# Kernel optimization log

Measured on AMD Instinct MI355X. Metric: run time of the kernel, lower is better.

Reference implementation:

```python
import jax, jax.numpy as jnp
import numpy as np

N_CLASSES = 16384
M = 2
D = 128


def setup_inputs() -> dict:
    key = jax.random.key(0)
    k1, k2 = jax.random.split(key)
    x = jax.random.normal(k1, (N_CLASSES * M, D), dtype=jnp.float32)
    anchor_idx = jax.random.randint(k2, (N_CLASSES,), 0, M, dtype=jnp.int64 if jax.config.jax_enable_x64 else jnp.int32).astype(jnp.int32)
    pos_idx = (1 - anchor_idx).astype(jnp.int32)  # randperm(2) -> positive is the other sample
    return {"x": x, "anchor_idx": anchor_idx, "pos_idx": pos_idx}


def reference(x, anchor_idx, pos_idx):
    # x: [N*M, D]; anchor_idx/pos_idx: [N] in [0, M)
    N = anchor_idx.shape[0]
    Dx = x.shape[1]
    xr = x.reshape(N, M, Dx)
    anchors = jnp.take_along_axis(xr, anchor_idx[:, None, None], axis=1)[:, 0, :]    # [N, D]
    positives = jnp.take_along_axis(xr, pos_idx[:, None, None], axis=1)[:, 0, :]     # [N, D]
    negs = xr[:, 1, :]                                                               # [N, D] (sample 1 of every class)
    # score[i, j] = a_i . (neg_j - pos_i) = a_i . neg_j - a_i . pos_i
    S = anchors @ negs.T                                                             # [N, N]
    ap = jnp.sum(anchors * positives, axis=1)                                        # [N]
    logits = S - ap[:, None]
    mask = ~jnp.eye(N, dtype=bool)                                                   # exclude j == i (own class)
    sums = jnp.sum(jnp.where(mask, jnp.exp(logits), jnp.float32(0.0)), axis=1)       # [N]
    return jnp.sum(jnp.log1p(sums))
```

## Files before the change

### kernel.cpp

```cpp
#include <hip/hip_runtime.h>
#include <hip/hip_bf16.h>
#include <math.h>

#define N_CLS 16384
#define DDIM  128
#define LOG2E 1.4426950408889634f

#if __has_builtin(__builtin_amdgcn_exp2f)
#define EXP2(x) __builtin_amdgcn_exp2f(x)
#else
#define EXP2(x) exp2f(x)
#endif

typedef __attribute__((ext_vector_type(8))) short short8;
typedef __attribute__((ext_vector_type(16))) float f32x16;

__device__ __forceinline__ unsigned short f2bf(float f) {
    __hip_bfloat16 h = __float2bfloat16(f);
    return *(unsigned short*)&h;
}

__global__ __launch_bounds__(256)
void prep_kernel(const float* __restrict__ x,
                 const int* __restrict__ aidx,
                 float* __restrict__ ap,
                 unsigned short* __restrict__ Afrag,
                 unsigned short* __restrict__ Bfrag,
                 float* __restrict__ out) {
    const int u  = blockIdx.x * 256 + threadIdx.x;
    const int i  = u >> 4;
    const int sl = u & 15;
    const int k0 = sl * 8;

    const float* pa = x + (2L * i) * DDIM + k0;
    float fa[8], fb[8];
    *(float4*)&fa[0] = *(const float4*)(pa);
    *(float4*)&fa[4] = *(const float4*)(pa + 4);
    *(float4*)&fb[0] = *(const float4*)(pa + DDIM);
    *(float4*)&fb[4] = *(const float4*)(pa + DDIM + 4);
    const bool sel = (aidx[i] != 0);

    short8 A, B;
    float d = 0.0f;
    #pragma unroll
    for (int j = 0; j < 8; ++j) {
        const float av = sel ? fb[j] : fa[j];
        A[j] = (short)f2bf(av * LOG2E);
        B[j] = (short)f2bf(fb[j]);
        d += fa[j] * fb[j];
    }
    const long dst = (long)(i >> 5) * 4096 + (sl >> 1) * 512 +
                     ((sl & 1) * 32 + (i & 31)) * 8;
    *(short8*)(Afrag + dst) = A;
    *(short8*)(Bfrag + dst) = B;

    d += __shfl_xor(d, 1, 64);
    d += __shfl_xor(d, 2, 64);
    d += __shfl_xor(d, 4, 64);
    d += __shfl_xor(d, 8, 64);
    if (sl == 0) ap[i] = d;
    if (u == 0) out[0] = 0.0f;
}

__global__ __launch_bounds__(256, 4)
void fused_kernel(const unsigned short* __restrict__ Afrag,
                  const unsigned short* __restrict__ Bfrag,
                  float* __restrict__ partial) {
    __shared__ __align__(16) unsigned short bs[2][4096];
    const int tid  = threadIdx.x;
    const int lane = tid & 63;
    const int w    = tid >> 6;
    const int l31  = lane & 31;
    const int hi   = lane >> 5;
    const int oct  = blockIdx.x & 7;
    const int rt   = blockIdx.x >> 3;
    const int gRow = rt * 4 + w;

    short8 af[8];
    {
        const unsigned short* a0 = Afrag + (long)gRow * 4096 + lane * 8;
        #pragma unroll
        for (int kc = 0; kc < 8; ++kc)
            af[kc] = *(const short8*)(a0 + kc * 512);
    }
    const unsigned short* bbase = Bfrag + (long)oct * (64L * 4096) + lane * 8;
    const int wchunk = w * 1024;

    int ctd = gRow - oct * 64;
    if (ctd < 0 || ctd >= 64) ctd = -1000;

    float rs[16];
    #pragma unroll
    for (int q = 0; q < 16; ++q) rs[q] = 0.0f;

    {
        short8 s0 = *(const short8*)(bbase + wchunk);
        short8 s1 = *(const short8*)(bbase + wchunk + 512);
        *(short8*)(&bs[0][wchunk + lane * 8]) = s0;
        *(short8*)(&bs[0][wchunk + 512 + lane * 8]) = s1;
    }
    __syncthreads();

    for (int ct = 0; ct < 64; ++ct) {
        const int cur = ct & 1;
        const long nt = (ct < 63) ? (long)(ct + 1) : 63L;
        short8 n0 = *(const short8*)(bbase + nt * 4096 + wchunk);
        short8 n1 = *(const short8*)(bbase + nt * 4096 + wchunk + 512);

        f32x16 acc;
        #pragma unroll
        for (int q = 0; q < 16; ++q) acc[q] = 0.0f;

        const unsigned short* bp = &bs[cur][lane * 8];
        __builtin_amdgcn_s_setprio(1);
        #pragma unroll
        for (int kc = 0; kc < 8; ++kc) {
            short8 b = *(const short8*)(bp + kc * 512);
            acc = __builtin_amdgcn_mfma_f32_32x32x16_bf16(af[kc], b, acc, 0, 0, 0);
        }
        __builtin_amdgcn_s_setprio(0);

        if (ct == ctd) {
            #pragma unroll
            for (int q = 0; q < 16; ++q) {
                const float e = EXP2(acc[q]);
                const int row = (q & 3) + 8 * (q >> 2) + 4 * hi;
                rs[q] += (l31 == row) ? 0.0f : e;
            }
        } else {
            #pragma unroll
            for (int q = 0; q < 16; ++q) rs[q] += EXP2(acc[q]);
        }

        *(short8*)(&bs[cur ^ 1][wchunk + lane * 8]) = n0;
        *(short8*)(&bs[cur ^ 1][wchunk + 512 + lane * 8]) = n1;
        __syncthreads();
    }

    #pragma unroll
    for (int q = 0; q < 16; ++q) {
        float v = rs[q];
        v += __shfl_xor(v, 1, 64);
        v += __shfl_xor(v, 2, 64);
        v += __shfl_xor(v, 4, 64);
        v += __shfl_xor(v, 8, 64);
        v += __shfl_xor(v, 16, 64);
        if (l31 == 0) {
            const int row = (q & 3) + 8 * (q >> 2) + 4 * hi;
            partial[(long)oct * N_CLS + (long)gRow * 32 + row] = v;
        }
    }
}

__global__ __launch_bounds__(256)
void finalize_kernel(const float* __restrict__ partial,
                     const float* __restrict__ ap,
                     float* __restrict__ out) {
    __shared__ float red[256];
    const int t = threadIdx.x;
    const int row = blockIdx.x * 256 + t;
    float s = 0.0f;
    #pragma unroll
    for (int p = 0; p < 8; ++p) s += partial[(long)p * N_CLS + row];
    const float u = logf(s) - ap[row];
    const float loss = (u > 25.0f) ? u : log1pf(__expf(u));
    red[t] = loss;
    __syncthreads();
    for (int st = 128; st > 0; st >>= 1) {
        if (t < st) red[t] += red[t + st];
        __syncthreads();
    }
    if (t == 0) atomicAdd(out, red[0]);
}

extern "C" void kernel_launch(void* const* d_in, const int* in_sizes, int n_in,
                              void* d_out, int out_size, void* d_ws, size_t ws_size,
                              hipStream_t stream) {
    const float* x    = (const float*)d_in[0];
    const int*   aidx = (const int*)d_in[1];

    char* ws = (char*)d_ws;
    float* ap             = (float*)(ws);
    float* partial        = (float*)(ws + 131072);
    unsigned short* Afrag = (unsigned short*)(ws + 131072 + 1048576);
    unsigned short* Bfrag = (unsigned short*)(ws + 131072 + 1048576 + 4194304);

    prep_kernel<<<1024, 256, 0, stream>>>(x, aidx, ap, Afrag, Bfrag, (float*)d_out);
    fused_kernel<<<1024, 256, 0, stream>>>(Afrag, Bfrag, partial);
    finalize_kernel<<<64, 256, 0, stream>>>(partial, ap, (float*)d_out);
}
```

Before: 143.9 us.

## Split waves into MFMA producers and exp consumers with LDS handoff

Inside each block, waves are split into producer waves that run the MFMA tiles for two row tiles each and consumer waves that read the accumulators from LDS and do the exp2 and row-sum work one tile behind. The aim is to overlap the matrix-core work with the transcendental and VALU epilogue, which previously ran serially within each wave. In exchange it adds an LDS round trip for the accumulators, an extra block barrier per tile, and halves the number of waves issuing MFMAs. Producer and consumer roles alternate across block halves to balance the load on each SIMD.

```diff
diff --git a/kernel.cpp b/kernel.cpp
--- a/kernel.cpp
+++ b/kernel.cpp
@@ -13,6 +13,7 @@
 #endif
 
 typedef __attribute__((ext_vector_type(8))) short short8;
+typedef __attribute__((ext_vector_type(4)))  float f32x4;
 typedef __attribute__((ext_vector_type(16))) float f32x16;
 
 __device__ __forceinline__ unsigned short f2bf(float f) {
@@ -67,87 +68,125 @@
                   const unsigned short* __restrict__ Bfrag,
                   float* __restrict__ partial) {
     __shared__ __align__(16) unsigned short bs[2][4096];
+    __shared__ __align__(16) float accb[4][1024];
     const int tid  = threadIdx.x;
     const int lane = tid & 63;
     const int w    = tid >> 6;
     const int l31  = lane & 31;
     const int hi   = lane >> 5;
     const int oct  = blockIdx.x & 7;
-    const int rt   = blockIdx.x >> 3;
-    const int gRow = rt * 4 + w;
-
-    short8 af[8];
+    const int rg   = blockIdx.x >> 3;
+    const int rbit = (blockIdx.x >> 8) & 1;
+    const bool isP = (((w >> 1) ^ rbit) & 1) == 0;
+    const int pair = w & 1;
+    const int gRow0 = rg * 4 + pair * 2;
+    const int gRow1 = gRow0 + 1;
+    const int wchunk = w * 1024;
+
+    const unsigned short* bbase = Bfrag + (long)oct * (64L * 4096);
+
+    int ctd0 = gRow0 - oct * 64;
+    int ctd1 = gRow1 - oct * 64;
+    if (ctd0 < 0 || ctd0 >= 64) ctd0 = -1000;
+    if (ctd1 < 0 || ctd1 >= 64) ctd1 = -1000;
+
+    short8 af0[8], af1[8];
+    if (isP) {
+        const unsigned short* a0 = Afrag + (long)gRow0 * 4096 + lane * 8;
+        const unsigned short* a1 = Afrag + (long)gRow1 * 4096 + lane * 8;
+        #pragma unroll
+        for (int kc = 0; kc < 8; ++kc) {
+            af0[kc] = *(const short8*)(a0 + kc * 512);
+            af1[kc] = *(const short8*)(a1 + kc * 512);
+        }
+    }
+    f32x16 acc0, acc1;
+
+    float rs0[16], rs1[16];
+    #pragma unroll
+    for (int q = 0; q < 16; ++q) { rs0[q] = 0.0f; rs1[q] = 0.0f; }
+
+    const float* ab0 = accb[pair * 2];
+    const float* ab1 = accb[pair * 2 + 1];
+
+    auto consume = [&](int ct) {
+        #pragma unroll
+        for (int g = 0; g < 4; ++g) {
+            f32x4 v0 = *(const f32x4*)(ab0 + g * 256 + lane * 4);
+            f32x4 v1 = *(const f32x4*)(ab1 + g * 256 + lane * 4);
+            #pragma unroll
+            for (int j = 0; j < 4; ++j) {
+                const int row = j + 8 * g + 4 * hi;
+                float e0 = EXP2(v0[j]);
+                float e1 = EXP2(v1[j]);
+                if (ct == ctd0 && l31 == row) e0 = 0.0f;
+                if (ct == ctd1 && l31 == row) e1 = 0.0f;
+                rs0[g * 4 + j] += e0;
+                rs1[g * 4 + j] += e1;
+            }
+        }
+    };
+
     {
-        const unsigned short* a0 = Afrag + (long)gRow * 4096 + lane * 8;
-        #pragma unroll
-        for (int kc = 0; kc < 8; ++kc)
-            af[kc] = *(const short8*)(a0 + kc * 512);
-    }
-    const unsigned short* bbase = Bfrag + (long)oct * (64L * 4096) + lane * 8;
-    const int wchunk = w * 1024;
-
-    int ctd = gRow - oct * 64;
-    if (ctd < 0 || ctd >= 64) ctd = -1000;
-
-    float rs[16];
-    #pragma unroll
-    for (int q = 0; q < 16; ++q) rs[q] = 0.0f;
-
-    {
-        short8 s0 = *(const short8*)(bbase + wchunk);
-        short8 s1 = *(const short8*)(bbase + wchunk + 512);
+        short8 s0 = *(const short8*)(bbase + wchunk + lane * 8);
+        short8 s1 = *(const short8*)(bbase + wchunk + 512 + lane * 8);
         *(short8*)(&bs[0][wchunk + lane * 8]) = s0;
         *(short8*)(&bs[0][wchunk + 512 + lane * 8]) = s1;
     }
     __syncthreads();
 
-    for (int ct = 0; ct < 64; ++ct) {
-        const int cur = ct & 1;
-        const long nt = (ct < 63) ? (long)(ct + 1) : 63L;
-        short8 n0 = *(const short8*)(bbase + nt * 4096 + wchunk);
-        short8 n1 = *(const short8*)(bbase + nt * 4096 + wchunk + 512);
-
-        f32x16 acc;
-        #pragma unroll
-        for (int q = 0; q < 16; ++q) acc[q] = 0.0f;
-
-        const unsigned short* bp = &bs[cur][lane * 8];
-        __builtin_amdgcn_s_setprio(1);
-        #pragma unroll
-        for (int kc = 0; kc < 8; ++kc) {
-            short8 b = *(const short8*)(bp + kc * 512);
-            acc = __builtin_amdgcn_mfma_f32_32x32x16_bf16(af[kc], b, acc, 0, 0, 0);
-        }
-        __builtin_amdgcn_s_setprio(0);
-
-        if (ct == ctd) {
-            #pragma unroll
-            for (int q = 0; q < 16; ++q) {
-                const float e = EXP2(acc[q]);
-                const int row = (q & 3) + 8 * (q >> 2) + 4 * hi;
-                rs[q] += (l31 == row) ? 0.0f : e;
-            }
-        } else {
-            #pragma unroll
-            for (int q = 0; q < 16; ++q) rs[q] += EXP2(acc[q]);
-        }
+    for (int t = 0; t < 64; ++t) {
+        const int cur = t & 1;
+        const long ntile = (t < 63) ? (long)(t + 1) : 63L;
+        short8 n0 = *(const short8*)(bbase + ntile * 4096 + wchunk + lane * 8);
+        short8 n1 = *(const short8*)(bbase + ntile * 4096 + wchunk + 512 + lane * 8);
+
+        if (isP) {
+            #pragma unroll
+            for (int q = 0; q < 16; ++q) { acc0[q] = 0.0f; acc1[q] = 0.0f; }
+            const unsigned short* bp = &bs[cur][lane * 8];
+            __builtin_amdgcn_s_setprio(1);
+            #pragma unroll
+            for (int kc = 0; kc < 8; ++kc) {
+                short8 b = *(const short8*)(bp + kc * 512);
+                acc0 = __builtin_amdgcn_mfma_f32_32x32x16_bf16(af0[kc], b, acc0, 0, 0, 0);
+                acc1 = __builtin_amdgcn_mfma_f32_32x32x16_bf16(af1[kc], b, acc1, 0, 0, 0);
+            }
+            __builtin_amdgcn_s_setprio(0);
+        } else if (t > 0) {
+            consume(t - 1);
+        }
+        __syncthreads();
 
         *(short8*)(&bs[cur ^ 1][wchunk + lane * 8]) = n0;
         *(short8*)(&bs[cur ^ 1][wchunk + 512 + lane * 8]) = n1;
+        if (isP) {
+            #pragma unroll
+            for (int g = 0; g < 4; ++g) {
+                *(f32x4*)(ab0 + g * 256 + lane * 4) =
+                    (f32x4){acc0[g*4], acc0[g*4+1], acc0[g*4+2], acc0[g*4+3]};
+                *(f32x4*)(ab1 + g * 256 + lane * 4) =
+                    (f32x4){acc1[g*4], acc1[g*4+1], acc1[g*4+2], acc1[g*4+3]};
+            }
+        }
         __syncthreads();
     }
 
-    #pragma unroll
-    for (int q = 0; q < 16; ++q) {
-        float v = rs[q];
-        v += __shfl_xor(v, 1, 64);
-        v += __shfl_xor(v, 2, 64);
-        v += __shfl_xor(v, 4, 64);
-        v += __shfl_xor(v, 8, 64);
-        v += __shfl_xor(v, 16, 64);
-        if (l31 == 0) {
-            const int row = (q & 3) + 8 * (q >> 2) + 4 * hi;
-            partial[(long)oct * N_CLS + (long)gRow * 32 + row] = v;
+    if (!isP) {
+        consume(63);
+        #pragma unroll
+        for (int q = 0; q < 16; ++q) {
+            float v0 = rs0[q], v1 = rs1[q];
+            v0 += __shfl_xor(v0, 1, 64);  v1 += __shfl_xor(v1, 1, 64);
+            v0 += __shfl_xor(v0, 2, 64);  v1 += __shfl_xor(v1, 2, 64);
+            v0 += __shfl_xor(v0, 4, 64);  v1 += __shfl_xor(v1, 4, 64);
+            v0 += __shfl_xor(v0, 8, 64);  v1 += __shfl_xor(v1, 8, 64);
+            v0 += __shfl_xor(v0, 16, 64); v1 += __shfl_xor(v1, 16, 64);
+            if (l31 == 0) {
+                const int row = (q & 3) + 8 * (q >> 2) + 4 * hi;
+                partial[(long)oct * N_CLS + (long)gRow0 * 32 + row] = v0;
+                partial[(long)oct * N_CLS + (long)gRow1 * 32 + row] = v1;
+            }
         }
     }
 }
```

Result: slower. 219.2 us (+52.3%).
